# Kernel tuning notes

Measured on AMD Instinct MI355X. Metric: run time of the kernel, lower is better.

## Reference

```python
import jax, jax.numpy as jnp
import numpy as np

B, L, D, H = 4, 1024, 1024, 16
DH = D // H
NEG = -1e9
EPS = 1e-5


def setup_inputs() -> dict:
    key = jax.random.key(0)
    ks = jax.random.split(key, 12)
    s = 1.0 / np.sqrt(D)
    inp = {
        "Q": jax.random.normal(ks[0], (B, L, D), jnp.float32),
        "K": jax.random.normal(ks[1], (B, L, D), jnp.float32),
        "V": jax.random.normal(ks[2], (B, L, D), jnp.float32),
        "K_mask": jnp.ones((B, L), jnp.int32),
        "WQ": jax.random.normal(ks[3], (D, D), jnp.float32) * s,
        "bQ": jnp.zeros((D,), jnp.float32),
        "WK": jax.random.normal(ks[4], (D, D), jnp.float32) * s,
        "bK": jnp.zeros((D,), jnp.float32),
        "WV": jax.random.normal(ks[5], (D, D), jnp.float32) * s,
        "bV": jnp.zeros((D,), jnp.float32),
        "WO": jax.random.normal(ks[6], (D, D), jnp.float32) * s,
        "bO": jnp.zeros((D,), jnp.float32),
        "ln_g": jnp.ones((D,), jnp.float32),
        "ln_b": jnp.zeros((D,), jnp.float32),
    }
    return inp


def _mha(Q, K, V, K_mask, WQ, bQ, WK, bK, WV, bV, WO, bO, ln_g, ln_b):
    # projections  [B,L,D]
    q = Q @ WQ + bQ
    k = K @ WK + bK
    v = V @ WV + bV
    # split heads -> [B,H,L,dh]
    q = q.reshape(B, L, H, DH).transpose(0, 2, 1, 3)
    k = k.reshape(B, L, H, DH).transpose(0, 2, 1, 3)
    v = v.reshape(B, L, H, DH).transpose(0, 2, 1, 3)
    # scaled dot product, masked softmax over keys
    scores = jnp.einsum("bhqd,bhkd->bhqk", q, k) / jnp.sqrt(jnp.float32(DH))
    mask = (K_mask > 0)[:, None, None, :]  # [B,1,1,Lk]
    scores = jnp.where(mask, scores, NEG)
    attn = jax.nn.softmax(scores, axis=-1)  # dropout is identity at inference
    ctx = jnp.einsum("bhqk,bhkd->bhqd", attn, v)
    ctx = ctx.transpose(0, 2, 1, 3).reshape(B, L, D)
    # output layer: dense + residual + layernorm
    out = ctx @ WO + bO
    x = out + Q
    mu = jnp.mean(x, axis=-1, keepdims=True)
    var = jnp.var(x, axis=-1, keepdims=True)
    return (x - mu) * jax.lax.rsqrt(var + EPS) * ln_g + ln_b


def reference(Q, K, V, K_mask, WQ, bQ, WK, bK, WV, bV, WO, bO, ln_g, ln_b):
    return _mha(Q, K, V, K_mask, WQ, bQ, WK, bK, WV, bV, WO, bO, ln_g, ln_b)
```

## Files before the change

kernel.cpp:

```cpp
#include <hip/hip_runtime.h>
#include <hip/hip_bf16.h>
#include <stdint.h>

#define Bn 4
#define Ln 1024
#define Dn 1024
#define Hn 16
#define DHn 64
#define Mn (Bn*Ln)

typedef __attribute__((ext_vector_type(8))) short short8v;
typedef __attribute__((ext_vector_type(4))) float floatx4;

__device__ __forceinline__ unsigned short f2b(float f){
  union { float f; unsigned u; } v; v.f = f;
  unsigned r = (v.u + 0x7FFFu + ((v.u >> 16) & 1u)) >> 16;
  return (unsigned short)r;
}
__device__ __forceinline__ unsigned short f2b_fast(float f){
  __hip_bfloat16 h = __float2bfloat16(f);
  return *reinterpret_cast<unsigned short*>(&h);
}

typedef const unsigned __attribute__((address_space(1)))* gas1_t;
typedef unsigned __attribute__((address_space(3)))* las3_t;
__device__ __forceinline__ void gload16(const void* g, void* l){
  __builtin_amdgcn_global_load_lds((gas1_t)(uintptr_t)g, (las3_t)(uintptr_t)l, 16, 0, 0);
}

__global__ __launch_bounds__(256) void tobf16x3_k(const float* __restrict__ x0,
    const float* __restrict__ x1, const float* __restrict__ x2,
    unsigned short* __restrict__ o0, unsigned short* __restrict__ o1,
    unsigned short* __restrict__ o2)
{
  const int i = blockIdx.x * 256 + threadIdx.x;
  const int sel = i >> 20, idx = i & 0xFFFFF;
  const float* x = sel == 0 ? x0 : (sel == 1 ? x1 : x2);
  unsigned short* o = sel == 0 ? o0 : (sel == 1 ? o1 : o2);
  float4 v = reinterpret_cast<const float4*>(x)[idx];
  union { unsigned short u[4]; uint2 q; } p;
  p.u[0] = f2b(v.x); p.u[1] = f2b(v.y); p.u[2] = f2b(v.z); p.u[3] = f2b(v.w);
  reinterpret_cast<uint2*>(o)[idx] = p.q;
}

__global__ __launch_bounds__(256) void wconv4_k(const float* __restrict__ W0,
    const float* __restrict__ W1, const float* __restrict__ W2,
    const float* __restrict__ W3, unsigned short* __restrict__ Wt0,
    unsigned short* __restrict__ Wt1, unsigned short* __restrict__ Wt2,
    unsigned short* __restrict__ Wt3)
{
  const float* W; unsigned short* Wt;
  switch (blockIdx.z){
    case 0: W = W0; Wt = Wt0; break;
    case 1: W = W1; Wt = Wt1; break;
    case 2: W = W2; Wt = Wt2; break;
    default: W = W3; Wt = Wt3; break;
  }
  __shared__ float tile[64][65];
  const int nb = blockIdx.x * 64, kb = blockIdx.y * 64;
  const int tx = threadIdx.x & 63, ty = threadIdx.x >> 6;
  #pragma unroll
  for (int r = 0; r < 64; r += 4)
    tile[r + ty][tx] = W[(size_t)(kb + r + ty) * 1024 + nb + tx];
  __syncthreads();
  #pragma unroll
  for (int r = 0; r < 64; r += 4)
    Wt[(size_t)(nb + r + ty) * 1024 + kb + tx] = f2b(tile[tx][r + ty]);
}

template<int MODE>
__device__ __forceinline__ void gemm_core(const unsigned short* __restrict__ Ab,
    const unsigned short* __restrict__ Btp, const float* __restrict__ bias,
    void* __restrict__ outp, const float* __restrict__ resid, float scale,
    unsigned short* lds, int nt, int mt)
{
  const int tid = threadIdx.x;
  const int lane = tid & 63, wave = tid >> 6;
  const int wr = wave >> 1, wc = wave & 1;
  const int lg = lane >> 4, lr = lane & 15;
  const int m0 = mt * 128, n0 = nt * 128;

  const unsigned short* gA[4];
  const unsigned short* gB[4];
  #pragma unroll
  for (int i = 0; i < 4; i++){
    int c = (wave * 4 + i) * 64 + lane;
    int ks = c >> 9, r16 = (c >> 6) & 7, lhi = (c >> 4) & 3, lrr = c & 15;
    int row = r16 * 16 + lrr, col = ks * 32 + lhi * 8;
    gA[i] = Ab  + (size_t)(m0 + row) * 1024 + col;
    gB[i] = Btp + (size_t)(n0 + row) * 1024 + col;
  }

  floatx4 acc[4][4] = {};

  auto issue = [&](int t){
    unsigned short* bufA = lds + (t % 3) * 16384;
    unsigned short* bufB = bufA + 8192;
    #pragma unroll
    for (int i = 0; i < 4; i++){
      gload16(gA[i] + t * 64, &bufA[(wave * 4 + i) * 512]);
      gload16(gB[i] + t * 64, &bufB[(wave * 4 + i) * 512]);
    }
  };

  issue(0);
  issue(1);

  for (int kb = 0; kb < 16; kb++){
    unsigned short* bufA = lds + (kb % 3) * 16384;
    unsigned short* bufB = bufA + 8192;
    if (kb < 14){
      issue(kb + 2);
      asm volatile("s_waitcnt vmcnt(16)" ::: "memory");
    } else if (kb == 14){
      asm volatile("s_waitcnt vmcnt(8)" ::: "memory");
    } else {
      asm volatile("s_waitcnt vmcnt(0)" ::: "memory");
    }
    __builtin_amdgcn_s_barrier();
    __builtin_amdgcn_sched_barrier(0);
    #pragma unroll
    for (int ks = 0; ks < 2; ks++){
      short8v af[4], bfr[4];
      #pragma unroll
      for (int m = 0; m < 4; m++)
        af[m] = *reinterpret_cast<const short8v*>(&bufA[((ks * 8 + wr * 4 + m) * 64 + lane) * 8]);
      #pragma unroll
      for (int n = 0; n < 4; n++)
        bfr[n] = *reinterpret_cast<const short8v*>(&bufB[((ks * 8 + wc * 4 + n) * 64 + lane) * 8]);
      #pragma unroll
      for (int m = 0; m < 4; m++)
        #pragma unroll
        for (int n = 0; n < 4; n++)
          acc[m][n] = __builtin_amdgcn_mfma_f32_16x16x32_bf16(af[m], bfr[n], acc[m][n], 0, 0, 0);
    }
    __builtin_amdgcn_sched_barrier(0);
    __builtin_amdgcn_s_barrier();
  }

  if constexpr (MODE == 2){
    __syncthreads();
    #pragma unroll
    for (int n = 0; n < 4; n++){
      const int gn_l = wc * 64 + n * 16 + lr;
      const float bb = bias[n0 + gn_l];
      const int X = (gn_l & 7) << 3;
      #pragma unroll
      for (int m = 0; m < 4; m++){
        const int gm_l = wr * 64 + m * 16 + lg * 4;
        union { unsigned short u[4]; uint2 q; } pk;
        #pragma unroll
        for (int r = 0; r < 4; r++) pk.u[r] = f2b((acc[m][n][r] + bb) * scale);
        *reinterpret_cast<uint2*>(&lds[gn_l * 128 + (gm_l ^ X)]) = pk.q;
      }
    }
    __syncthreads();
    const int b = m0 >> 10, l0 = m0 & 1023;
    const int row = tid >> 1, colb = (tid & 1) * 64;
    const int h2 = (n0 + row) >> 6, d = (n0 + row) & 63;
    unsigned short* obase = (unsigned short*)outp +
        (((size_t)(b * Hn + h2)) * DHn + d) * Ln + l0 + colb;
    const int XR = (row & 7) << 3;
    #pragma unroll
    for (int g = 0; g < 8; g++){
      short8v v = *reinterpret_cast<const short8v*>(&lds[row * 128 + ((colb + g * 8) ^ XR)]);
      *reinterpret_cast<short8v*>(obase + g * 8) = v;
    }
  } else {
    #pragma unroll
    for (int n = 0; n < 4; n++){
      const int gn = n0 + wc * 64 + n * 16 + lr;
      const float bb = bias[gn];
      #pragma unroll
      for (int m = 0; m < 4; m++){
        const int gm0 = m0 + wr * 64 + m * 16 + lg * 4;
        #pragma unroll
        for (int r = 0; r < 4; r++){
          const int gm = gm0 + r;
          float v = (acc[m][n][r] + bb) * scale;
          if constexpr (MODE == 0){
            unsigned short* o = (unsigned short*)outp;
            int b = gm >> 10, l = gm & 1023, h2 = gn >> 6, d = gn & 63;
            o[(((size_t)(b * Hn + h2)) * Ln + l) * DHn + d] = f2b(v);
          } else {
            float* o = (float*)outp;
            o[(size_t)gm * Dn + gn] = v + resid[(size_t)gm * Dn + gn];
          }
        }
      }
    }
  }
}

__global__ __launch_bounds__(256) void gemmqkv_k(
    const unsigned short* __restrict__ A0, const unsigned short* __restrict__ A1,
    const unsigned short* __restrict__ A2, const unsigned short* __restrict__ W0,
    const unsigned short* __restrict__ W1, const unsigned short* __restrict__ W2,
    const float* __restrict__ b0, const float* __restrict__ b1,
    const float* __restrict__ b2, unsigned short* __restrict__ o0,
    unsigned short* __restrict__ o1, unsigned short* __restrict__ o2, float qscl)
{
  __shared__ __align__(16) unsigned short lds[49152];
  const int bid = blockIdx.x;
  const int xcd = bid & 7, k = bid >> 3;
  const int panel = xcd * 12 + (k >> 3);
  const int nt = k & 7;
  const int mt = panel & 31, z = panel >> 5;
  if (z == 0)
    gemm_core<0>(A0, W0, b0, o0, nullptr, qscl, lds, nt, mt);
  else if (z == 1)
    gemm_core<0>(A1, W1, b1, o1, nullptr, 1.f, lds, nt, mt);
  else
    gemm_core<2>(A2, W2, b2, o2, nullptr, 1.f, lds, nt, mt);
}

__global__ __launch_bounds__(256) void gemmo_k(const unsigned short* __restrict__ Ab,
    const unsigned short* __restrict__ W, const float* __restrict__ bias,
    float* __restrict__ out, const float* __restrict__ resid)
{
  __shared__ __align__(16) unsigned short lds[49152];
  const int bid = blockIdx.x;
  const int xcd = bid & 7, k = bid >> 3;
  const int mt = xcd * 4 + (k >> 3);
  const int nt = k & 7;
  gemm_core<3>(Ab, W, bias, out, resid, 1.f, lds, nt, mt);
}

__global__ __launch_bounds__(256) void attn_k(const unsigned short* __restrict__ qb,
    const unsigned short* __restrict__ kbf, const unsigned short* __restrict__ vtb,
    const int* __restrict__ kmask, unsigned short* __restrict__ ctx)
{
  const int bh = blockIdx.x;
  const int qt = blockIdx.y;
  const int b = bh >> 4, h = bh & 15;
  const int tid = threadIdx.x;
  const int w = tid >> 6, lane = tid & 63;
  const int lg = lane >> 4, lr = lane & 15;

  const unsigned short* qp = qb  + (size_t)bh * Ln * DHn;
  const unsigned short* kp = kbf + (size_t)bh * Ln * DHn;
  const unsigned short* vp = vtb + (size_t)bh * DHn * Ln;
  const int q0 = qt * 128 + w * 32;

  __shared__ __align__(16) unsigned short ldsK[2][4096];
  __shared__ __align__(16) unsigned short ldsV[2][4096];
  __shared__ __align__(16) unsigned short plds[4][32][72];

  const unsigned short* gK[2];
  const unsigned short* gV[2];
  #pragma unroll
  for (int i = 0; i < 2; i++){
    int bc = w * 2 + i;
    int ks = bc >> 2, j = bc & 3;
    int row = j * 16 + lr, col = ks * 32 + lg * 8;
    gK[i] = kp + (size_t)row * DHn + col;
    gV[i] = vp + (size_t)row * Ln  + col;
  }

  short8v aq[2][2];
  #pragma unroll
  for (int f = 0; f < 2; f++)
    #pragma unroll
    for (int ks = 0; ks < 2; ks++)
      aq[f][ks] = *reinterpret_cast<const short8v*>(
          qp + (size_t)(q0 + f * 16 + lr) * DHn + ks * 32 + lg * 8);

  floatx4 accO[2][4] = {};
  float lsacc[2][4] = {{0.f,0.f,0.f,0.f},{0.f,0.f,0.f,0.f}};

  const int* mrow = kmask + b * Ln;
  int mkA[4], mkB[4];

  #pragma unroll
  for (int i = 0; i < 2; i++){
    gload16(gK[i], &ldsK[0][(w * 2 + i) * 512]);
    gload16(gV[i], &ldsV[0][(w * 2 + i) * 512]);
  }
  #pragma unroll
  for (int j = 0; j < 4; j++) mkA[j] = mrow[j * 16 + lr];

  for (int t = 0; t < 16; t++){
    const int cur = t & 1;
    asm volatile("s_waitcnt vmcnt(0)" ::: "memory");
    __syncthreads();
    if (t < 15){
      #pragma unroll
      for (int i = 0; i < 2; i++){
        gload16(gK[i] + (size_t)(t + 1) * 4096, &ldsK[cur ^ 1][(w * 2 + i) * 512]);
        gload16(gV[i] + (size_t)(t + 1) * 64,   &ldsV[cur ^ 1][(w * 2 + i) * 512]);
      }
      #pragma unroll
      for (int j = 0; j < 4; j++) mkB[j] = mrow[(t + 1) * 64 + j * 16 + lr];
    }

    floatx4 s[2][4] = {};
    #pragma unroll
    for (int ks = 0; ks < 2; ks++)
      #pragma unroll
      for (int j = 0; j < 4; j++){
        short8v bk = *reinterpret_cast<const short8v*>(&ldsK[cur][((ks * 4 + j) * 64 + lane) * 8]);
        s[0][j] = __builtin_amdgcn_mfma_f32_16x16x32_bf16(aq[0][ks], bk, s[0][j], 0, 0, 0);
        s[1][j] = __builtin_amdgcn_mfma_f32_16x16x32_bf16(aq[1][ks], bk, s[1][j], 0, 0, 0);
      }
    if (__all(mkA[0] > 0 && mkA[1] > 0 && mkA[2] > 0 && mkA[3] > 0)){
      #pragma unroll
      for (int f = 0; f < 2; f++)
        #pragma unroll
        for (int j = 0; j < 4; j++)
          #pragma unroll
          for (int r = 0; r < 4; r++){
            float p = __builtin_amdgcn_exp2f(s[f][j][r]);
            lsacc[f][r] += p;
            plds[w][f * 16 + lg * 4 + r][j * 16 + lr] = f2b_fast(p);
          }
    } else {
      #pragma unroll
      for (int j = 0; j < 4; j++){
        const float madd = mkA[j] > 0 ? 0.f : -1e9f;
        #pragma unroll
        for (int f = 0; f < 2; f++)
          #pragma unroll
          for (int r = 0; r < 4; r++){
            float p = __builtin_amdgcn_exp2f(s[f][j][r] + madd);
            lsacc[f][r] += p;
            plds[w][f * 16 + lg * 4 + r][j * 16 + lr] = f2b_fast(p);
          }
      }
    }
    #pragma unroll
    for (int ks = 0; ks < 2; ks++){
      short8v pa0 = *reinterpret_cast<const short8v*>(&plds[w][lr][ks * 32 + lg * 8]);
      short8v pa1 = *reinterpret_cast<const short8v*>(&plds[w][16 + lr][ks * 32 + lg * 8]);
      #pragma unroll
      for (int n = 0; n < 4; n++){
        short8v bv = *reinterpret_cast<const short8v*>(&ldsV[cur][((ks * 4 + n) * 64 + lane) * 8]);
        accO[0][n] = __builtin_amdgcn_mfma_f32_16x16x32_bf16(pa0, bv, accO[0][n], 0, 0, 0);
        accO[1][n] = __builtin_amdgcn_mfma_f32_16x16x32_bf16(pa1, bv, accO[1][n], 0, 0, 0);
      }
    }
    #pragma unroll
    for (int j = 0; j < 4; j++) mkA[j] = mkB[j];
  }

  #pragma unroll
  for (int f = 0; f < 2; f++)
    #pragma unroll
    for (int r = 0; r < 4; r++){
      lsacc[f][r] += __shfl_xor(lsacc[f][r], 1, 64);
      lsacc[f][r] += __shfl_xor(lsacc[f][r], 2, 64);
      lsacc[f][r] += __shfl_xor(lsacc[f][r], 4, 64);
      lsacc[f][r] += __shfl_xor(lsacc[f][r], 8, 64);
      lsacc[f][r] = 1.f / fmaxf(lsacc[f][r], 1e-20f);
    }
  #pragma unroll
  for (int f = 0; f < 2; f++)
    #pragma unroll
    for (int n = 0; n < 4; n++)
      #pragma unroll
      for (int r = 0; r < 4; r++){
        float o = accO[f][n][r] * lsacc[f][r];
        int q = q0 + f * 16 + lg * 4 + r;
        ctx[((size_t)(b * Ln + q)) * Dn + h * DHn + n * 16 + lr] = f2b_fast(o);
      }
}

__global__ __launch_bounds__(256) void ln_k(const float* __restrict__ x,
    const float* __restrict__ g, const float* __restrict__ bt, float* __restrict__ out)
{
  const int row = blockIdx.x;
  const int tid = threadIdx.x;
  float4 v = *reinterpret_cast<const float4*>(x + (size_t)row * 1024 + tid * 4);
  float s  = v.x + v.y + v.z + v.w;
  float sq = v.x * v.x + v.y * v.y + v.z * v.z + v.w * v.w;
  #pragma unroll
  for (int off = 32; off >= 1; off >>= 1){
    s  += __shfl_xor(s, off, 64);
    sq += __shfl_xor(sq, off, 64);
  }
  __shared__ float psm[4], pqm[4];
  const int w = tid >> 6;
  if ((tid & 63) == 0){ psm[w] = s; pqm[w] = sq; }
  __syncthreads();
  s  = psm[0] + psm[1] + psm[2] + psm[3];
  sq = pqm[0] + pqm[1] + pqm[2] + pqm[3];
  const float mean = s * (1.f / 1024.f);
  const float var  = sq * (1.f / 1024.f) - mean * mean;
  const float inv  = rsqrtf(var + 1e-5f);
  float4 gg = *reinterpret_cast<const float4*>(g  + tid * 4);
  float4 bb = *reinterpret_cast<const float4*>(bt + tid * 4);
  float4 o;
  o.x = (v.x - mean) * inv * gg.x + bb.x;
  o.y = (v.y - mean) * inv * gg.y + bb.y;
  o.z = (v.z - mean) * inv * gg.z + bb.z;
  o.w = (v.w - mean) * inv * gg.w + bb.w;
  *reinterpret_cast<float4*>(out + (size_t)row * 1024 + tid * 4) = o;
}

extern "C" void kernel_launch(void* const* d_in, const int* in_sizes, int n_in,
                              void* d_out, int out_size, void* d_ws, size_t ws_size,
                              hipStream_t stream)
{
  const float* Qin = (const float*)d_in[0];
  const float* Kin = (const float*)d_in[1];
  const float* Vin = (const float*)d_in[2];
  const int*   Kms = (const int*)d_in[3];
  const float* WQ  = (const float*)d_in[4];
  const float* bQ  = (const float*)d_in[5];
  const float* WK  = (const float*)d_in[6];
  const float* bK  = (const float*)d_in[7];
  const float* WV  = (const float*)d_in[8];
  const float* bV  = (const float*)d_in[9];
  const float* WO  = (const float*)d_in[10];
  const float* bO  = (const float*)d_in[11];
  const float* lng = (const float*)d_in[12];
  const float* lnb = (const float*)d_in[13];

  char* ws = (char*)d_ws;
  const size_t MB = 1024u * 1024u;
  unsigned short* wqt = (unsigned short*)(ws + 0 * MB);
  unsigned short* wkt = (unsigned short*)(ws + 2 * MB);
  unsigned short* wvt = (unsigned short*)(ws + 4 * MB);
  unsigned short* wot = (unsigned short*)(ws + 6 * MB);
  unsigned short* qbf = (unsigned short*)(ws + 8 * MB);
  unsigned short* kbf = (unsigned short*)(ws + 16 * MB);
  unsigned short* vtb = (unsigned short*)(ws + 24 * MB);
  unsigned short* ctx = (unsigned short*)(ws + 32 * MB);
  float*          xbf = (float*)(ws + 40 * MB);
  unsigned short* cv0 = (unsigned short*)(ws + 32 * MB);
  unsigned short* cv1 = (unsigned short*)(ws + 40 * MB);
  unsigned short* cv2 = (unsigned short*)(ws + 48 * MB);

  dim3 blk(256);
  wconv4_k<<<dim3(16, 16, 4), blk, 0, stream>>>(WQ, WK, WV, WO, wqt, wkt, wvt, wot);
  tobf16x3_k<<<12288, blk, 0, stream>>>(Qin, Kin, Vin, cv0, cv1, cv2);

  const float QSCL = 0.125f * 1.44269504088896f;
  gemmqkv_k<<<768, blk, 0, stream>>>(cv0, cv1, cv2, wqt, wkt, wvt,
                                     bQ, bK, bV, qbf, kbf, vtb, QSCL);

  attn_k<<<dim3(64, 8), blk, 0, stream>>>(qbf, kbf, vtb, Kms, ctx);

  gemmo_k<<<256, blk, 0, stream>>>(ctx, wot, bO, xbf, Qin);

  ln_k<<<4096, blk, 0, stream>>>(xbf, lng, lnb, (float*)d_out);
}
```

Baseline: 137.5 us.

## Use 256x256 tiles with 8 waves for fused QKV projection GEMM

Replaces the 128x128, 4-wave QKV GEMM with a 256x256, 8-wave variant. It uses a 4-slot half-K-step LDS pipeline whose A and B stage loads are interleaved with the MFMA groups, plus s_setprio around the MFMAs. The larger tile raises arithmetic intensity and cuts global/L2 traffic per FLOP. In exchange the grid shrinks to 192 blocks, fewer than the 256 CUs, so some CUs sit idle, and register pressure rises with 32 accumulators per lane. The output GEMM is split into its own non-templated core.

```diff
diff --git a/kernel.cpp b/kernel.cpp
--- a/kernel.cpp
+++ b/kernel.cpp
@@ -69,9 +69,182 @@
 }
 
 template<int MODE>
-__device__ __forceinline__ void gemm_core(const unsigned short* __restrict__ Ab,
+__device__ __forceinline__ void gemm8_core(const unsigned short* __restrict__ Ab,
     const unsigned short* __restrict__ Btp, const float* __restrict__ bias,
-    void* __restrict__ outp, const float* __restrict__ resid, float scale,
+    void* __restrict__ outp, float scale, unsigned short* lds, int nt, int mt)
+{
+  const int tid = threadIdx.x;
+  const int lane = tid & 63, wave = tid >> 6;
+  const int wr = wave >> 2, wc = wave & 3;
+  const int lg = lane >> 4, lr = lane & 15;
+  const int m0 = mt * 256, n0 = nt * 256;
+
+  const unsigned short* gAb[2];
+  const unsigned short* gBb[2];
+  int ldso[2];
+  #pragma unroll
+  for (int i = 0; i < 2; i++){
+    int c = tid + 512 * i;
+    int g16 = c >> 6, lrr = c & 15, lgg = (c >> 4) & 3;
+    int row = g16 * 16 + lrr;
+    gAb[i] = Ab  + (size_t)(m0 + row) * 1024 + lgg * 8;
+    gBb[i] = Btp + (size_t)(n0 + row) * 1024 + lgg * 8;
+    ldso[i] = c * 8;
+  }
+  auto stageA = [&](int sg){
+    unsigned short* slot = lds + (sg & 3) * 16384;
+    const int kcol = (sg >> 1) * 64 + (sg & 1) * 32;
+    #pragma unroll
+    for (int i = 0; i < 2; i++) gload16(gAb[i] + kcol, &slot[ldso[i]]);
+  };
+  auto stageB = [&](int sg){
+    unsigned short* slot = lds + (sg & 3) * 16384 + 8192;
+    const int kcol = (sg >> 1) * 64 + (sg & 1) * 32;
+    #pragma unroll
+    for (int i = 0; i < 2; i++) gload16(gBb[i] + kcol, &slot[ldso[i]]);
+  };
+
+  floatx4 acc[8][4] = {};
+
+  stageA(0); stageB(0); stageA(1); stageB(1); stageA(2); stageB(2);
+
+  for (int t = 0; t < 16; t++){
+    unsigned short* slot0 = lds + ((2 * t) & 3) * 16384;
+    unsigned short* slot1 = lds + ((2 * t + 1) & 3) * 16384;
+    short8v af[4], bf[4];
+    if (t < 15) asm volatile("s_waitcnt vmcnt(4)" ::: "memory");
+    else        asm volatile("s_waitcnt vmcnt(0)" ::: "memory");
+    __builtin_amdgcn_s_barrier();
+    __builtin_amdgcn_sched_barrier(0);
+    if (t < 15) stageA(2 * t + 3);
+    #pragma unroll
+    for (int n = 0; n < 4; n++)
+      bf[n] = *reinterpret_cast<const short8v*>(&slot0[8192 + ((wc * 4 + n) * 64 + lane) * 8]);
+    #pragma unroll
+    for (int i2 = 0; i2 < 4; i2++)
+      af[i2] = *reinterpret_cast<const short8v*>(&slot0[((wr * 8 + i2) * 64 + lane) * 8]);
+    __builtin_amdgcn_s_setprio(1);
+    #pragma unroll
+    for (int a = 0; a < 4; a++)
+      #pragma unroll
+      for (int n = 0; n < 4; n++)
+        acc[a][n] = __builtin_amdgcn_mfma_f32_16x16x32_bf16(af[a], bf[n], acc[a][n], 0, 0, 0);
+    __builtin_amdgcn_s_setprio(0);
+    if (t < 15) stageB(2 * t + 3);
+    #pragma unroll
+    for (int i2 = 0; i2 < 4; i2++)
+      af[i2] = *reinterpret_cast<const short8v*>(&slot0[((wr * 8 + 4 + i2) * 64 + lane) * 8]);
+    __builtin_amdgcn_s_setprio(1);
+    #pragma unroll
+    for (int a = 0; a < 4; a++)
+      #pragma unroll
+      for (int n = 0; n < 4; n++)
+        acc[4 + a][n] = __builtin_amdgcn_mfma_f32_16x16x32_bf16(af[a], bf[n], acc[4 + a][n], 0, 0, 0);
+    __builtin_amdgcn_s_setprio(0);
+    __builtin_amdgcn_sched_barrier(0);
+    __builtin_amdgcn_s_barrier();
+    __builtin_amdgcn_sched_barrier(0);
+    if (t < 14) stageA(2 * t + 4);
+    #pragma unroll
+    for (int n = 0; n < 4; n++)
+      bf[n] = *reinterpret_cast<const short8v*>(&slot1[8192 + ((wc * 4 + n) * 64 + lane) * 8]);
+    #pragma unroll
+    for (int i2 = 0; i2 < 4; i2++)
+      af[i2] = *reinterpret_cast<const short8v*>(&slot1[((wr * 8 + i2) * 64 + lane) * 8]);
+    __builtin_amdgcn_s_setprio(1);
+    #pragma unroll
+    for (int a = 0; a < 4; a++)
+      #pragma unroll
+      for (int n = 0; n < 4; n++)
+        acc[a][n] = __builtin_amdgcn_mfma_f32_16x16x32_bf16(af[a], bf[n], acc[a][n], 0, 0, 0);
+    __builtin_amdgcn_s_setprio(0);
+    if (t < 14) stageB(2 * t + 4);
+    #pragma unroll
+    for (int i2 = 0; i2 < 4; i2++)
+      af[i2] = *reinterpret_cast<const short8v*>(&slot1[((wr * 8 + 4 + i2) * 64 + lane) * 8]);
+    __builtin_amdgcn_s_setprio(1);
+    #pragma unroll
+    for (int a = 0; a < 4; a++)
+      #pragma unroll
+      for (int n = 0; n < 4; n++)
+        acc[4 + a][n] = __builtin_amdgcn_mfma_f32_16x16x32_bf16(af[a], bf[n], acc[4 + a][n], 0, 0, 0);
+    __builtin_amdgcn_s_setprio(0);
+    __builtin_amdgcn_sched_barrier(0);
+  }
+
+  if constexpr (MODE == 2){
+    __syncthreads();
+    #pragma unroll
+    for (int n = 0; n < 4; n++){
+      const int gn_l = wc * 64 + n * 16 + lr;
+      const float bb = bias[n0 + gn_l];
+      const int X = (gn_l & 7) << 3;
+      #pragma unroll
+      for (int a = 0; a < 8; a++){
+        const int gm_l = wr * 128 + a * 16 + lg * 4;
+        union { unsigned short u[4]; uint2 q; } pk;
+        #pragma unroll
+        for (int r = 0; r < 4; r++) pk.u[r] = f2b((acc[a][n][r] + bb) * scale);
+        *reinterpret_cast<uint2*>(&lds[gn_l * 256 + (gm_l ^ X)]) = pk.q;
+      }
+    }
+    __syncthreads();
+    const int bb2 = m0 >> 10, l0 = m0 & 1023;
+    const int row = tid >> 1, colb = (tid & 1) * 128;
+    const int h2 = (n0 + row) >> 6, d = (n0 + row) & 63;
+    unsigned short* obase = (unsigned short*)outp +
+        (((size_t)(bb2 * Hn + h2)) * DHn + d) * Ln + l0 + colb;
+    const int XR = (row & 7) << 3;
+    #pragma unroll
+    for (int g = 0; g < 16; g++){
+      short8v v = *reinterpret_cast<const short8v*>(&lds[row * 256 + ((colb + g * 8) ^ XR)]);
+      *reinterpret_cast<short8v*>(obase + g * 8) = v;
+    }
+  } else {
+    unsigned short* o = (unsigned short*)outp;
+    #pragma unroll
+    for (int n = 0; n < 4; n++){
+      const int gn = n0 + wc * 64 + n * 16 + lr;
+      const float bbv = bias[gn];
+      const int h2 = gn >> 6, d = gn & 63;
+      #pragma unroll
+      for (int a = 0; a < 8; a++){
+        const int gm0v = m0 + wr * 128 + a * 16 + lg * 4;
+        #pragma unroll
+        for (int r = 0; r < 4; r++){
+          const int gm = gm0v + r;
+          const int bb2 = gm >> 10, l = gm & 1023;
+          o[(((size_t)(bb2 * Hn + h2)) * Ln + l) * DHn + d] = f2b((acc[a][n][r] + bbv) * scale);
+        }
+      }
+    }
+  }
+}
+
+__global__ __launch_bounds__(512, 2) void gemmqkv8_k(
+    const unsigned short* __restrict__ A0, const unsigned short* __restrict__ A1,
+    const unsigned short* __restrict__ A2, const unsigned short* __restrict__ W0,
+    const unsigned short* __restrict__ W1, const unsigned short* __restrict__ W2,
+    const float* __restrict__ b0, const float* __restrict__ b1,
+    const float* __restrict__ b2, unsigned short* __restrict__ o0,
+    unsigned short* __restrict__ o1, unsigned short* __restrict__ o2, float qscl)
+{
+  __shared__ __align__(16) unsigned short lds[65536];
+  const int g = blockIdx.x >> 3;
+  const int nt = g & 3;
+  const int panel = (g >> 2) * 8 + (blockIdx.x & 7);
+  const int z = panel >> 4, mt = panel & 15;
+  if (z == 0)
+    gemm8_core<0>(A0, W0, b0, o0, qscl, lds, nt, mt);
+  else if (z == 1)
+    gemm8_core<0>(A1, W1, b1, o1, 1.f, lds, nt, mt);
+  else
+    gemm8_core<2>(A2, W2, b2, o2, 1.f, lds, nt, mt);
+}
+
+__device__ __forceinline__ void gemm_core3(const unsigned short* __restrict__ Ab,
+    const unsigned short* __restrict__ Btp, const float* __restrict__ bias,
+    float* __restrict__ outp, const float* __restrict__ resid,
     unsigned short* lds, int nt, int mt)
 {
   const int tid = threadIdx.x;
@@ -103,8 +276,7 @@
     }
   };
 
-  issue(0);
-  issue(1);
+  issue(0); issue(1);
 
   for (int kb = 0; kb < 16; kb++){
     unsigned short* bufA = lds + (kb % 3) * 16384;
@@ -138,80 +310,21 @@
     __builtin_amdgcn_s_barrier();
   }
 
-  if constexpr (MODE == 2){
-    __syncthreads();
-    #pragma unroll
-    for (int n = 0; n < 4; n++){
-      const int gn_l = wc * 64 + n * 16 + lr;
-      const float bb = bias[n0 + gn_l];
-      const int X = (gn_l & 7) << 3;
-      #pragma unroll
-      for (int m = 0; m < 4; m++){
-        const int gm_l = wr * 64 + m * 16 + lg * 4;
-        union { unsigned short u[4]; uint2 q; } pk;
-        #pragma unroll
-        for (int r = 0; r < 4; r++) pk.u[r] = f2b((acc[m][n][r] + bb) * scale);
-        *reinterpret_cast<uint2*>(&lds[gn_l * 128 + (gm_l ^ X)]) = pk.q;
-      }
-    }
-    __syncthreads();
-    const int b = m0 >> 10, l0 = m0 & 1023;
-    const int row = tid >> 1, colb = (tid & 1) * 64;
-    const int h2 = (n0 + row) >> 6, d = (n0 + row) & 63;
-    unsigned short* obase = (unsigned short*)outp +
-        (((size_t)(b * Hn + h2)) * DHn + d) * Ln + l0 + colb;
-    const int XR = (row & 7) << 3;
-    #pragma unroll
-    for (int g = 0; g < 8; g++){
-      short8v v = *reinterpret_cast<const short8v*>(&lds[row * 128 + ((colb + g * 8) ^ XR)]);
-      *reinterpret_cast<short8v*>(obase + g * 8) = v;
-    }
-  } else {
-    #pragma unroll
-    for (int n = 0; n < 4; n++){
-      const int gn = n0 + wc * 64 + n * 16 + lr;
-      const float bb = bias[gn];
-      #pragma unroll
-      for (int m = 0; m < 4; m++){
-        const int gm0 = m0 + wr * 64 + m * 16 + lg * 4;
-        #pragma unroll
-        for (int r = 0; r < 4; r++){
-          const int gm = gm0 + r;
-          float v = (acc[m][n][r] + bb) * scale;
-          if constexpr (MODE == 0){
-            unsigned short* o = (unsigned short*)outp;
-            int b = gm >> 10, l = gm & 1023, h2 = gn >> 6, d = gn & 63;
-            o[(((size_t)(b * Hn + h2)) * Ln + l) * DHn + d] = f2b(v);
-          } else {
-            float* o = (float*)outp;
-            o[(size_t)gm * Dn + gn] = v + resid[(size_t)gm * Dn + gn];
-          }
-        }
-      }
-    }
-  }
-}
-
-__global__ __launch_bounds__(256) void gemmqkv_k(
-    const unsigned short* __restrict__ A0, const unsigned short* __restrict__ A1,
-    const unsigned short* __restrict__ A2, const unsigned short* __restrict__ W0,
-    const unsigned short* __restrict__ W1, const unsigned short* __restrict__ W2,
-    const float* __restrict__ b0, const float* __restrict__ b1,
-    const float* __restrict__ b2, unsigned short* __restrict__ o0,
-    unsigned short* __restrict__ o1, unsigned short* __restrict__ o2, float qscl)
-{
-  __shared__ __align__(16) unsigned short lds[49152];
-  const int bid = blockIdx.x;
-  const int xcd = bid & 7, k = bid >> 3;
-  const int panel = xcd * 12 + (k >> 3);
-  const int nt = k & 7;
-  const int mt = panel & 31, z = panel >> 5;
-  if (z == 0)
-    gemm_core<0>(A0, W0, b0, o0, nullptr, qscl, lds, nt, mt);
-  else if (z == 1)
-    gemm_core<0>(A1, W1, b1, o1, nullptr, 1.f, lds, nt, mt);
-  else
-    gemm_core<2>(A2, W2, b2, o2, nullptr, 1.f, lds, nt, mt);
+  #pragma unroll
+  for (int n = 0; n < 4; n++){
+    const int gn = n0 + wc * 64 + n * 16 + lr;
+    const float bb = bias[gn];
+    #pragma unroll
+    for (int m = 0; m < 4; m++){
+      const int gm0 = m0 + wr * 64 + m * 16 + lg * 4;
+      #pragma unroll
+      for (int r = 0; r < 4; r++){
+        const int gm = gm0 + r;
+        float v = acc[m][n][r] + bb;
+        outp[(size_t)gm * Dn + gn] = v + resid[(size_t)gm * Dn + gn];
+      }
+    }
+  }
 }
 
 __global__ __launch_bounds__(256) void gemmo_k(const unsigned short* __restrict__ Ab,
@@ -223,7 +336,7 @@
   const int xcd = bid & 7, k = bid >> 3;
   const int mt = xcd * 4 + (k >> 3);
   const int nt = k & 7;
-  gemm_core<3>(Ab, W, bias, out, resid, 1.f, lds, nt, mt);
+  gemm_core3(Ab, W, bias, out, resid, lds, nt, mt);
 }
 
 __global__ __launch_bounds__(256) void attn_k(const unsigned short* __restrict__ qb,
@@ -435,8 +548,8 @@
   tobf16x3_k<<<12288, blk, 0, stream>>>(Qin, Kin, Vin, cv0, cv1, cv2);
 
   const float QSCL = 0.125f * 1.44269504088896f;
-  gemmqkv_k<<<768, blk, 0, stream>>>(cv0, cv1, cv2, wqt, wkt, wvt,
-                                     bQ, bK, bV, qbf, kbf, vtb, QSCL);
+  gemmqkv8_k<<<192, dim3(512), 0, stream>>>(cv0, cv1, cv2, wqt, wkt, wvt,
+                                            bQ, bK, bV, qbf, kbf, vtb, QSCL);
 
   attn_k<<<dim3(64, 8), blk, 0, stream>>>(qbf, kbf, vtb, Kms, ctx);
 
```

Result: faster. 120.3 us (-12.5%).
